# Performance work log

Measured on AMD Instinct MI355X. Metric: run time of the kernel, lower is better.

## Reference

```python
import jax, jax.numpy as jnp
import numpy as np

# Representative causal-LM config (pre-LN GPT/Llama-style, eager attention)
L, D, H, FF, V = 2, 2048, 16, 8192, 32000
B, S = 2, 1024
DH = D // H
NEG = -1e9


def setup_inputs() -> dict:
    key = jax.random.key(0)
    ks = jax.random.split(key, 10)
    p = lambda k, shape: jax.random.normal(k, shape, dtype=jnp.float32) * 0.02
    return {
        "input_ids": jax.random.randint(ks[0], (B, S), 0, V),
        "attention_mask": jnp.ones((B, S), dtype=jnp.int32),
        "emb": p(ks[1], (V, D)),
        "ln1_g": jnp.ones((L, D)), "ln1_b": jnp.zeros((L, D)),
        "Wqkv": p(ks[2], (L, D, 3 * D)),
        "Wo": p(ks[3], (L, D, D)),
        "ln2_g": jnp.ones((L, D)), "ln2_b": jnp.zeros((L, D)),
        "W1": p(ks[4], (L, D, FF)), "W2": p(ks[5], (L, FF, D)),
        "lnf_g": jnp.ones((D,)), "lnf_b": jnp.zeros((D,)),
        "Wc1": p(ks[6], (D, D)), "bc1": jnp.zeros((D,)),
        "Wc2": p(ks[7], (D, 2)), "bc2": jnp.zeros((2,)),
    }


def _ln(x, g, b):
    m = x.mean(-1, keepdims=True)
    v = ((x - m) ** 2).mean(-1, keepdims=True)
    return (x - m) * jax.lax.rsqrt(v + 1e-5) * g + b


def _transformer_reward(input_ids, attention_mask, emb, ln1_g, ln1_b, Wqkv, Wo,
                        ln2_g, ln2_b, W1, W2, lnf_g, lnf_b, Wc1, bc1, Wc2, bc2):
    x = emb[input_ids]                                  # [B,S,D] embedding lookup
    causal = jnp.tril(jnp.ones((S, S), dtype=bool))     # [S,S]
    pad = attention_mask.astype(bool)[:, None, None, :] # [B,1,1,S]
    bias = jnp.where(causal[None, None] & pad, 0.0, NEG).astype(jnp.float32)
    scale = 1.0 / np.sqrt(DH).astype(np.float32)
    for l in range(L):
        h = _ln(x, ln1_g[l], ln1_b[l])
        qkv = h @ Wqkv[l]                               # [B,S,3D]
        q, k, v = jnp.split(qkv, 3, axis=-1)
        q = q.reshape(B, S, H, DH).transpose(0, 2, 1, 3)
        k = k.reshape(B, S, H, DH).transpose(0, 2, 1, 3)
        v = v.reshape(B, S, H, DH).transpose(0, 2, 1, 3)
        # eager attention: full [B,H,S,S] score matrix (as in attn_implementation='eager')
        scores = jnp.einsum('bhqd,bhkd->bhqk', q, k) * scale + bias
        attn = jax.nn.softmax(scores, axis=-1)
        o = jnp.einsum('bhqk,bhkd->bhqd', attn, v).transpose(0, 2, 1, 3).reshape(B, S, D)
        x = x + o @ Wo[l]
        h = _ln(x, ln2_g[l], ln2_b[l])
        x = x + jax.nn.gelu(h @ W1[l]) @ W2[l]
    hs = _ln(x, lnf_g, lnf_b)                           # hidden_states[-1]
    m = attention_mask[:, :, None].astype(jnp.float32)
    mean = (hs * m).sum(axis=1) / jnp.clip(m.sum(axis=1), 1e-9)  # masked mean pool
    logits = jnp.tanh(mean @ Wc1 + bc1) @ Wc2 + bc2     # classifier head
    return jax.nn.softmax(logits, axis=-1)[:, 1]        # rewards [B]


def reference(input_ids, attention_mask, emb, ln1_g, ln1_b, Wqkv, Wo,
              ln2_g, ln2_b, W1, W2, lnf_g, lnf_b, Wc1, bc1, Wc2, bc2):
    return _transformer_reward(input_ids, attention_mask, emb, ln1_g, ln1_b, Wqkv, Wo,
                               ln2_g, ln2_b, W1, W2, lnf_g, lnf_b, Wc1, bc1, Wc2, bc2)
```

## Files before the change

kernel.cpp:

```cpp
#include <hip/hip_runtime.h>
#include <hip/hip_bf16.h>

using bf16 = __hip_bfloat16;
typedef short s16x8 __attribute__((ext_vector_type(8)));
typedef float f32x4 __attribute__((ext_vector_type(4)));

static constexpr int D  = 2048;
static constexpr int H  = 16;
static constexpr int FF = 8192;
static constexpr int S  = 1024;
static constexpr int NB = 2;
static constexpr int DH = 128;
static constexpr int L  = 2;
static constexpr int BS = NB * S;
static constexpr int BH = NB * H;
static constexpr int D3 = 3 * D;

__device__ __forceinline__ float wave_sum(float v) {
#pragma unroll
  for (int o = 32; o > 0; o >>= 1) v += __shfl_down(v, o, 64);
  return v;
}
__device__ __forceinline__ float wave_max(float v) {
#pragma unroll
  for (int o = 32; o > 0; o >>= 1) v = fmaxf(v, __shfl_down(v, o, 64));
  return v;
}

__device__ __forceinline__ void gll16(const void* g, void* l) {
  __builtin_amdgcn_global_load_lds(
      (const __attribute__((address_space(1))) unsigned int*)g,
      (__attribute__((address_space(3))) unsigned int*)l, 16, 0, 0);
}

__device__ __forceinline__ float gelu_tanh(float x) {
  return 0.5f * x * (1.0f + tanhf(0.7978845608028654f * (x + 0.044715f * x * x * x)));
}

__device__ __forceinline__ void stv(float* p, long i, float v) { p[i] = v; }
__device__ __forceinline__ void stv(bf16* p, long i, float v)  { p[i] = __float2bfloat16(v); }

template <int EPI>
__launch_bounds__(256)
__global__ void gemm_k(const bf16* __restrict__ A, int lda, long sAb, long sAh,
                       const bf16* __restrict__ Bt, int ldb, long sBb, long sBh,
                       void* __restrict__ Cp, int ldc, long sCb, long sCh,
                       const float* __restrict__ resid, int K, int nH) {
  __shared__ __align__(16) bf16 lsA[2][128 * 32];
  __shared__ __align__(16) bf16 lsB[2][128 * 32];
  const int tid = threadIdx.x;
  const int zb = blockIdx.z / nH, zh = blockIdx.z % nH;
  const int m0 = blockIdx.y * 128, n0 = blockIdx.x * 128;
  const int sr = tid >> 2, sc = (tid & 3) * 8;
  const bf16* Ag = A + zb * sAb + zh * sAh + (long)(m0 + sr) * lda + sc;
  const bf16* Bg = Bt + zb * sBb + zh * sBh + (long)(n0 + sr) * ldb + sc;
  const long a64 = 64L * lda, b64 = 64L * ldb;

  const int lane = tid & 63, wv = tid >> 6;
  const int wm = (wv >> 1) * 64, wn = (wv & 1) * 64;
  const int fl = lane & 15, fg = lane >> 4;

  f32x4 acc[4][4];
#pragma unroll
  for (int i = 0; i < 4; i++)
#pragma unroll
    for (int j = 0; j < 4; j++) acc[i][j] = (f32x4){0.f, 0.f, 0.f, 0.f};

  gll16(Ag, lsA[0] + tid * 8);
  gll16(Ag + a64, lsA[0] + 2048 + tid * 8);
  gll16(Bg, lsB[0] + tid * 8);
  gll16(Bg + b64, lsB[0] + 2048 + tid * 8);
  __syncthreads();

  int it = 0;
  for (int k0 = 0; k0 < K; k0 += 32, it ^= 1) {
    const int nxt = it ^ 1;
    if (k0 + 32 < K) {
      gll16(Ag + k0 + 32, lsA[nxt] + tid * 8);
      gll16(Ag + a64 + k0 + 32, lsA[nxt] + 2048 + tid * 8);
      gll16(Bg + k0 + 32, lsB[nxt] + tid * 8);
      gll16(Bg + b64 + k0 + 32, lsB[nxt] + 2048 + tid * 8);
    }
    s16x8 af[4], bq[4];
#pragma unroll
    for (int i = 0; i < 4; i++) {
      af[i] = *(const s16x8*)(lsA[it] + (wm + i * 16 + fl) * 32 + fg * 8);
      bq[i] = *(const s16x8*)(lsB[it] + (wn + i * 16 + fl) * 32 + fg * 8);
    }
#pragma unroll
    for (int i = 0; i < 4; i++)
#pragma unroll
      for (int j = 0; j < 4; j++)
        acc[i][j] = __builtin_amdgcn_mfma_f32_16x16x32_bf16(af[i], bq[j], acc[i][j], 0, 0, 0);
    __syncthreads();
  }

  const long offC = zb * sCb + zh * sCh;
#pragma unroll
  for (int i = 0; i < 4; i++) {
#pragma unroll
    for (int j = 0; j < 4; j++) {
      const int row = m0 + wm + i * 16 + fg * 4;
      const int col = n0 + wn + j * 16 + fl;
#pragma unroll
      for (int r = 0; r < 4; r++) {
        const long ci = offC + (long)(row + r) * ldc + col;
        float v = acc[i][j][r];
        if (EPI == 0) {
          ((float*)Cp)[ci] = v;
        } else if (EPI == 1) {
          ((bf16*)Cp)[ci] = __float2bfloat16(v);
        } else if (EPI == 2) {
          ((float*)Cp)[ci] = v + resid[ci];
        } else {
          ((bf16*)Cp)[ci] = __float2bfloat16(gelu_tanh(v));
        }
      }
    }
  }
}

template <int EPI>
__launch_bounds__(512, 2)
__global__ void gemm256_k(const bf16* __restrict__ A, int lda, long sAb, long sAh,
                          const bf16* __restrict__ Bt, int ldb, long sBb, long sBh,
                          void* __restrict__ Cp, int ldc, long sCb, long sCh,
                          int K, int nH) {
  __shared__ __align__(16) bf16 lsA[2][256 * 64];
  __shared__ __align__(16) bf16 lsB[2][256 * 64];
  const int tid = threadIdx.x;
  const int zb = blockIdx.z / nH, zh = blockIdx.z % nH;
  const int m0 = blockIdx.y * 256, n0 = blockIdx.x * 256;

  const int sr = tid >> 3;
  const int sc = (tid & 7) ^ (sr & 7);
  const bf16* Ag = A + zb * sAb + zh * sAh + (long)(m0 + sr) * lda + sc * 8;
  const bf16* Bg = Bt + zb * sBb + zh * sBh +
                   (long)(n0 + (tid >> 8) * 64 + (sr & 31)) * ldb + sc * 8;

  const int lane = tid & 63, wv = tid >> 6;
  const int wm = wv >> 2;
  const int wn = wv & 3;
  const int fl = lane & 15, fg = lane >> 4;

  const int aob = (wm * 64 + fl) * 64;
  const int bob = (wn * 32 + fl) * 64;
  const int s0 = ((fg) ^ (fl & 7)) * 8;
  const int s1 = ((4 + fg) ^ (fl & 7)) * 8;

  s16x8 a[4][2];
  s16x8 bq[2][2][2];
  f32x4 acc[2][4][2][2];
#pragma unroll
  for (int qm = 0; qm < 2; qm++)
#pragma unroll
    for (int mf = 0; mf < 4; mf++)
#pragma unroll
      for (int qn = 0; qn < 2; qn++)
#pragma unroll
        for (int nf = 0; nf < 2; nf++) acc[qm][mf][qn][nf] = (f32x4){0.f, 0.f, 0.f, 0.f};

#define STAGE_A(buf, qm, kt)                                                  \
  do {                                                                        \
    const bf16* _s = Ag + (long)((qm) * 64) * lda + (kt) * 64;                \
    gll16(_s, lsA[buf] + (qm) * 8192 + tid * 8);                              \
    gll16(_s + 128L * lda, lsA[buf] + (qm) * 8192 + 4096 + tid * 8);          \
  } while (0)
#define STAGE_B(buf, qn, kt)                                                  \
  do {                                                                        \
    const bf16* _s = Bg + (long)((qn) * 32) * ldb + (kt) * 64;                \
    gll16(_s, lsB[buf] + (qn) * 8192 + tid * 8);                              \
    gll16(_s + 128L * ldb, lsB[buf] + (qn) * 8192 + 4096 + tid * 8);          \
  } while (0)
#define LDA8(buf, qm)                                                         \
  do {                                                                        \
    const bf16* _p = lsA[buf] + (qm) * 8192 + aob;                            \
    a[0][0] = *(const s16x8*)(_p + s0);        a[0][1] = *(const s16x8*)(_p + s1);        \
    a[1][0] = *(const s16x8*)(_p + 1024 + s0); a[1][1] = *(const s16x8*)(_p + 1024 + s1); \
    a[2][0] = *(const s16x8*)(_p + 2048 + s0); a[2][1] = *(const s16x8*)(_p + 2048 + s1); \
    a[3][0] = *(const s16x8*)(_p + 3072 + s0); a[3][1] = *(const s16x8*)(_p + 3072 + s1); \
  } while (0)
#define LDB4(buf, qn)                                                         \
  do {                                                                        \
    const bf16* _p = lsB[buf] + (qn) * 8192 + bob;                            \
    bq[qn][0][0] = *(const s16x8*)(_p + s0);        bq[qn][0][1] = *(const s16x8*)(_p + s1);        \
    bq[qn][1][0] = *(const s16x8*)(_p + 1024 + s0); bq[qn][1][1] = *(const s16x8*)(_p + 1024 + s1); \
  } while (0)
#define MM16(qm, qn)                                                          \
  do {                                                                        \
    _Pragma("unroll") for (int mf = 0; mf < 4; ++mf) {                        \
      acc[qm][mf][qn][0] = __builtin_amdgcn_mfma_f32_16x16x32_bf16(           \
          a[mf][0], bq[qn][0][0], acc[qm][mf][qn][0], 0, 0, 0);               \
      acc[qm][mf][qn][1] = __builtin_amdgcn_mfma_f32_16x16x32_bf16(           \
          a[mf][0], bq[qn][1][0], acc[qm][mf][qn][1], 0, 0, 0);               \
      acc[qm][mf][qn][0] = __builtin_amdgcn_mfma_f32_16x16x32_bf16(           \
          a[mf][1], bq[qn][0][1], acc[qm][mf][qn][0], 0, 0, 0);               \
      acc[qm][mf][qn][1] = __builtin_amdgcn_mfma_f32_16x16x32_bf16(           \
          a[mf][1], bq[qn][1][1], acc[qm][mf][qn][1], 0, 0, 0);               \
    }                                                                         \
  } while (0)
#define PHASE_TAIL(qm, qn)                                                    \
  __builtin_amdgcn_s_barrier();                                               \
  asm volatile("s_waitcnt lgkmcnt(0)" ::: "memory");                          \
  __builtin_amdgcn_sched_barrier(0);                                          \
  __builtin_amdgcn_s_setprio(1);                                              \
  MM16(qm, qn);                                                               \
  __builtin_amdgcn_s_setprio(0);

  const int NT = K >> 6;

  STAGE_A(0, 0, 0); STAGE_B(0, 0, 0); STAGE_B(0, 1, 0); STAGE_A(0, 1, 0);
  STAGE_A(1, 0, 1); STAGE_B(1, 0, 1); STAGE_B(1, 1, 1);
  asm volatile("s_waitcnt vmcnt(6)" ::: "memory");
  __builtin_amdgcn_s_barrier();

  for (int t = 0; t < NT; t += 2) {
    const bool nl = (t + 2 < NT);
    LDA8(0, 0);
    LDB4(0, 0);
    STAGE_A(1, 1, t + 1);
    PHASE_TAIL(0, 0);
    __builtin_amdgcn_s_barrier();
    LDB4(0, 1);
    if (nl) STAGE_A(0, 0, t + 2);
    PHASE_TAIL(0, 1);
    __builtin_amdgcn_s_barrier();
    LDA8(0, 1);
    if (nl) STAGE_B(0, 0, t + 2);
    PHASE_TAIL(1, 0);
    __builtin_amdgcn_s_barrier();
    if (nl) STAGE_B(0, 1, t + 2);
    PHASE_TAIL(1, 1);
    if (nl) asm volatile("s_waitcnt vmcnt(6)" ::: "memory");
    else    asm volatile("s_waitcnt vmcnt(0)" ::: "memory");
    __builtin_amdgcn_s_barrier();
    LDA8(1, 0);
    LDB4(1, 0);
    if (nl) STAGE_A(0, 1, t + 2);
    PHASE_TAIL(0, 0);
    __builtin_amdgcn_s_barrier();
    LDB4(1, 1);
    if (nl) STAGE_A(1, 0, t + 3);
    PHASE_TAIL(0, 1);
    __builtin_amdgcn_s_barrier();
    LDA8(1, 1);
    if (nl) STAGE_B(1, 0, t + 3);
    PHASE_TAIL(1, 0);
    __builtin_amdgcn_s_barrier();
    if (nl) STAGE_B(1, 1, t + 3);
    PHASE_TAIL(1, 1);
    if (nl) asm volatile("s_waitcnt vmcnt(6)" ::: "memory");
    __builtin_amdgcn_s_barrier();
  }

  const long offC = zb * sCb + zh * sCh;
#pragma unroll
  for (int qm = 0; qm < 2; qm++) {
#pragma unroll
    for (int mf = 0; mf < 4; mf++) {
#pragma unroll
      for (int qn = 0; qn < 2; qn++) {
#pragma unroll
        for (int nf = 0; nf < 2; nf++) {
          const int row = m0 + wm * 128 + qm * 64 + mf * 16 + fg * 4;
          const int col = n0 + wn * 64 + qn * 32 + nf * 16 + fl;
#pragma unroll
          for (int r = 0; r < 4; r++) {
            const long ci = offC + (long)(row + r) * ldc + col;
            float v = acc[qm][mf][qn][nf][r];
            if (EPI == 0) {
              ((float*)Cp)[ci] = v;
            } else if (EPI == 1) {
              ((bf16*)Cp)[ci] = __float2bfloat16(v);
            } else {
              ((bf16*)Cp)[ci] = __float2bfloat16(gelu_tanh(v));
            }
          }
        }
      }
    }
  }
#undef STAGE_A
#undef STAGE_B
#undef LDA8
#undef LDB4
#undef MM16
#undef PHASE_TAIL
}

__launch_bounds__(256)
__global__ void reduce4_k(const float* __restrict__ p, float* __restrict__ x) {
  const long i = (long)blockIdx.x * 256 + threadIdx.x;
  const long n = (long)BS * D / 4;
  const float4 a = ((const float4*)p)[i];
  const float4 b = ((const float4*)p)[i + n];
  const float4 c = ((const float4*)p)[i + 2 * n];
  const float4 d2 = ((const float4*)p)[i + 3 * n];
  float4 xv = ((float4*)x)[i];
  xv.x += a.x + b.x + c.x + d2.x;
  xv.y += a.y + b.y + c.y + d2.y;
  xv.z += a.z + b.z + c.z + d2.z;
  xv.w += a.w + b.w + c.w + d2.w;
  ((float4*)x)[i] = xv;
}

__launch_bounds__(256)
__global__ void transcast_k(const float* __restrict__ in, bf16* __restrict__ out,
                            int R, int C) {
  __shared__ float tile[32][33];
  const int tx = threadIdx.x, ty = threadIdx.y;
  const int c0 = blockIdx.x * 32, r0 = blockIdx.y * 32;
#pragma unroll
  for (int k = 0; k < 4; k++)
    tile[ty + 8 * k][tx] = in[(long)(r0 + ty + 8 * k) * C + c0 + tx];
  __syncthreads();
#pragma unroll
  for (int k = 0; k < 4; k++)
    out[(long)(c0 + ty + 8 * k) * R + r0 + tx] = __float2bfloat16(tile[tx][ty + 8 * k]);
}

__launch_bounds__(256)
__global__ void vtrans_k(const bf16* __restrict__ qkv, bf16* __restrict__ Vt) {
  __shared__ bf16 tile[32][33];
  const int z = blockIdx.z, b = z / H, h = z % H;
  const int d0 = blockIdx.x * 32, s0 = blockIdx.y * 32;
  const int tx = threadIdx.x, ty = threadIdx.y;
#pragma unroll
  for (int k = 0; k < 4; k++)
    tile[ty + 8 * k][tx] =
        qkv[(long)(b * S + s0 + ty + 8 * k) * D3 + 2 * D + h * DH + d0 + tx];
  __syncthreads();
#pragma unroll
  for (int k = 0; k < 4; k++)
    Vt[((long)z * DH + d0 + ty + 8 * k) * S + s0 + tx] = tile[tx][ty + 8 * k];
}

template <typename OutT>
__launch_bounds__(256)
__global__ void ln_k(const float* __restrict__ x, const float* __restrict__ g,
                     const float* __restrict__ bb, OutT* __restrict__ out) {
  __shared__ float sA[4], sB[4];
  const long row = blockIdx.x;
  const int tid = threadIdx.x;
  const float4* xr = (const float4*)(x + row * D);
  float4 v0 = xr[tid], v1 = xr[tid + 256];
  float s = v0.x + v0.y + v0.z + v0.w + v1.x + v1.y + v1.z + v1.w;
  float ss = v0.x * v0.x + v0.y * v0.y + v0.z * v0.z + v0.w * v0.w +
             v1.x * v1.x + v1.y * v1.y + v1.z * v1.z + v1.w * v1.w;
  s = wave_sum(s);
  ss = wave_sum(ss);
  const int lane = tid & 63, wv = tid >> 6;
  if (lane == 0) { sA[wv] = s; sB[wv] = ss; }
  __syncthreads();
  s = sA[0] + sA[1] + sA[2] + sA[3];
  ss = sB[0] + sB[1] + sB[2] + sB[3];
  const float mean = s * (1.f / D);
  const float var = ss * (1.f / D) - mean * mean;
  const float rstd = rsqrtf(var + 1e-5f);
  const float4* gv = (const float4*)g;
  const float4* bv = (const float4*)bb;
  float4 g0 = gv[tid], g1 = gv[tid + 256], c0 = bv[tid], c1 = bv[tid + 256];
  OutT* orow = out + row * D;
  stv(orow, 4 * tid + 0, (v0.x - mean) * rstd * g0.x + c0.x);
  stv(orow, 4 * tid + 1, (v0.y - mean) * rstd * g0.y + c0.y);
  stv(orow, 4 * tid + 2, (v0.z - mean) * rstd * g0.z + c0.z);
  stv(orow, 4 * tid + 3, (v0.w - mean) * rstd * g0.w + c0.w);
  stv(orow, 1024 + 4 * tid + 0, (v1.x - mean) * rstd * g1.x + c1.x);
  stv(orow, 1024 + 4 * tid + 1, (v1.y - mean) * rstd * g1.y + c1.y);
  stv(orow, 1024 + 4 * tid + 2, (v1.z - mean) * rstd * g1.z + c1.z);
  stv(orow, 1024 + 4 * tid + 3, (v1.w - mean) * rstd * g1.w + c1.w);
}

__launch_bounds__(256)
__global__ void embed_k(const int* __restrict__ ids, const float* __restrict__ emb,
                        float* __restrict__ x) {
  const long gid = (long)blockIdx.x * 256 + threadIdx.x;
  const int tok = (int)(gid >> 9);
  const int c = (int)(gid & 511);
  const int id = ids[tok];
  ((float4*)x)[gid] = ((const float4*)(emb + (long)id * D))[c];
}

__launch_bounds__(256)
__global__ void softmax_k(float* __restrict__ scores, const int* __restrict__ amask,
                          float scale) {
  __shared__ float sred[4];
  const int q = blockIdx.x, z = blockIdx.y, b = z / H;
  float* row = scores + ((long)z * S + q) * S;
  const int tid = threadIdx.x;
  const int lane = tid & 63, wv = tid >> 6;
  float v[4];
  float mx = -3.4e38f;
#pragma unroll
  for (int i = 0; i < 4; i++) {
    const int k = tid + i * 256;
    const float s = row[k] * scale;
    const bool ok = (k <= q) && (amask[b * S + k] != 0);
    v[i] = s + (ok ? 0.f : -1e9f);
    mx = fmaxf(mx, v[i]);
  }
  mx = wave_max(mx);
  if (lane == 0) sred[wv] = mx;
  __syncthreads();
  mx = fmaxf(fmaxf(sred[0], sred[1]), fmaxf(sred[2], sred[3]));
  __syncthreads();
  float e[4], sm = 0.f;
#pragma unroll
  for (int i = 0; i < 4; i++) {
    e[i] = __expf(v[i] - mx);
    sm += e[i];
  }
  sm = wave_sum(sm);
  if (lane == 0) sred[wv] = sm;
  __syncthreads();
  sm = sred[0] + sred[1] + sred[2] + sred[3];
  const float inv = 1.f / sm;
  bf16* orow = (bf16*)row;
#pragma unroll
  for (int i = 0; i < 4; i++) orow[tid + i * 256] = __float2bfloat16(e[i] * inv);
}

__launch_bounds__(256)
__global__ void pool_k(const float* __restrict__ hs, const int* __restrict__ amask,
                       float* __restrict__ pooled) {
  const int d = blockIdx.x * 256 + threadIdx.x;
  const int b = blockIdx.y;
  float s = 0.f, cnt = 0.f;
  for (int i = 0; i < S; i++) {
    const float m = (float)amask[b * S + i];
    s += hs[((long)(b * S + i)) * D + d] * m;
    cnt += m;
  }
  pooled[b * D + d] = s / fmaxf(cnt, 1e-9f);
}

__launch_bounds__(256)
__global__ void head1_k(const float* __restrict__ pooled, const float* __restrict__ Wc1,
                        const float* __restrict__ bc1, float* __restrict__ t) {
  const int j = blockIdx.x * 256 + threadIdx.x;
  const int b = blockIdx.y;
  float s = bc1[j];
  for (int d = 0; d < D; d++) s += pooled[b * D + d] * Wc1[(long)d * D + j];
  t[b * D + j] = tanhf(s);
}

__launch_bounds__(256)
__global__ void head2_k(const float* __restrict__ t, const float* __restrict__ Wc2,
                        const float* __restrict__ bc2, float* __restrict__ out) {
  __shared__ float red[4][4];
  const int tid = threadIdx.x;
  const int lane = tid & 63, wv = tid >> 6;
  float a[4] = {0.f, 0.f, 0.f, 0.f};
  for (int j = tid; j < D; j += 256) {
    const float w0 = Wc2[j * 2 + 0], w1 = Wc2[j * 2 + 1];
    const float t0 = t[j], t1 = t[D + j];
    a[0] += t0 * w0; a[1] += t0 * w1; a[2] += t1 * w0; a[3] += t1 * w1;
  }
#pragma unroll
  for (int c = 0; c < 4; c++) a[c] = wave_sum(a[c]);
  if (lane == 0) {
#pragma unroll
    for (int c = 0; c < 4; c++) red[wv][c] = a[c];
  }
  __syncthreads();
  if (tid == 0) {
    float tot[4];
#pragma unroll
    for (int c = 0; c < 4; c++) tot[c] = red[0][c] + red[1][c] + red[2][c] + red[3][c];
    const float l00 = tot[0] + bc2[0], l01 = tot[1] + bc2[1];
    const float l10 = tot[2] + bc2[0], l11 = tot[3] + bc2[1];
    out[0] = 1.f / (1.f + __expf(l00 - l01));
    out[1] = 1.f / (1.f + __expf(l10 - l11));
  }
}

extern "C" void kernel_launch(void* const* d_in, const int* in_sizes, int n_in,
                              void* d_out, int out_size, void* d_ws, size_t ws_size,
                              hipStream_t stream) {
  (void)in_sizes; (void)n_in; (void)out_size; (void)ws_size;
  const int*   ids   = (const int*)d_in[0];
  const int*   amask = (const int*)d_in[1];
  const float* emb   = (const float*)d_in[2];
  const float* ln1g  = (const float*)d_in[3];
  const float* ln1b  = (const float*)d_in[4];
  const float* Wqkv  = (const float*)d_in[5];
  const float* Wo    = (const float*)d_in[6];
  const float* ln2g  = (const float*)d_in[7];
  const float* ln2b  = (const float*)d_in[8];
  const float* W1    = (const float*)d_in[9];
  const float* W2    = (const float*)d_in[10];
  const float* lnfg  = (const float*)d_in[11];
  const float* lnfb  = (const float*)d_in[12];
  const float* Wc1   = (const float*)d_in[13];
  const float* bc1   = (const float*)d_in[14];
  const float* Wc2   = (const float*)d_in[15];
  const float* bc2   = (const float*)d_in[16];
  float* out = (float*)d_out;

  char* ws = (char*)d_ws;
  size_t off = 0;
  auto alloc = [&](size_t bytes) {
    size_t r = off;
    off += (bytes + 255) & ~(size_t)255;
    return r;
  };
  bf16* Wqkv_t = (bf16*)(ws + alloc((size_t)D3 * D * 2));
  bf16* Wo_t   = (bf16*)(ws + alloc((size_t)D * D * 2));
  bf16* W1_t   = (bf16*)(ws + alloc((size_t)FF * D * 2));
  bf16* W2_t   = (bf16*)(ws + alloc((size_t)D * FF * 2));
  float* x     = (float*)(ws + alloc((size_t)BS * D * 4));
  bf16* h      = (bf16*)(ws + alloc((size_t)BS * D * 2));
  bf16* qkv    = (bf16*)(ws + alloc((size_t)BS * D3 * 2));
  bf16* Vt     = (bf16*)(ws + alloc((size_t)BH * DH * S * 2));
  bf16* o_buf  = (bf16*)(ws + alloc((size_t)BS * D * 2));
  float* pooled= (float*)(ws + alloc((size_t)NB * D * 4));
  float* tb    = (float*)(ws + alloc((size_t)NB * D * 4));
  char* big    = ws + alloc((size_t)BH * S * S * 4);
  float* scores = (float*)big;
  bf16*  ffb    = (bf16*)big;
  float* hs     = (float*)big;
  float* parts  = (float*)(big + ((size_t)BS * FF * 2 + 255 & ~(size_t)255));

  const float scale = 0.088388347648318447f;
  dim3 blk(256);
  dim3 blk5(512);
  dim3 tblk(32, 8);

  embed_k<<<4096, blk, 0, stream>>>(ids, emb, x);

  for (int l = 0; l < L; l++) {
    transcast_k<<<dim3(D3 / 32, D / 32), tblk, 0, stream>>>(Wqkv + (size_t)l * D * D3, Wqkv_t, D, D3);
    transcast_k<<<dim3(D / 32, D / 32), tblk, 0, stream>>>(Wo + (size_t)l * D * D, Wo_t, D, D);
    transcast_k<<<dim3(FF / 32, D / 32), tblk, 0, stream>>>(W1 + (size_t)l * D * FF, W1_t, D, FF);
    transcast_k<<<dim3(D / 32, FF / 32), tblk, 0, stream>>>(W2 + (size_t)l * FF * D, W2_t, FF, D);

    ln_k<bf16><<<BS, blk, 0, stream>>>(x, ln1g + (size_t)l * D, ln1b + (size_t)l * D, h);
    gemm256_k<1><<<dim3(D3 / 256, BS / 256, 1), blk5, 0, stream>>>(
        h, D, 0, 0, Wqkv_t, D, 0, 0, qkv, D3, 0, 0, D, 1);
    vtrans_k<<<dim3(DH / 32, S / 32, BH), tblk, 0, stream>>>(qkv, Vt);
    gemm_k<0><<<dim3(S / 128, S / 128, BH), blk, 0, stream>>>(
        qkv, D3, (long)S * D3, DH,
        qkv + D, D3, (long)S * D3, DH,
        scores, S, (long)H * S * S, (long)S * S, nullptr, DH, H);
    softmax_k<<<dim3(S, BH), blk, 0, stream>>>(scores, amask, scale);
    gemm_k<1><<<dim3(DH / 128, S / 128, BH), blk, 0, stream>>>(
        (const bf16*)scores, 2 * S, (long)H * 2 * S * S, (long)2 * S * S,
        Vt, S, (long)H * DH * S, (long)DH * S,
        o_buf, D, (long)S * D, DH, nullptr, S, H);
    gemm_k<2><<<dim3(D / 128, BS / 128, 1), blk, 0, stream>>>(
        o_buf, D, 0, 0, Wo_t, D, 0, 0, x, D, 0, 0, x, D, 1);
    ln_k<bf16><<<BS, blk, 0, stream>>>(x, ln2g + (size_t)l * D, ln2b + (size_t)l * D, h);
    gemm256_k<3><<<dim3(FF / 256, BS / 256, 1), blk5, 0, stream>>>(
        h, D, 0, 0, W1_t, D, 0, 0, ffb, FF, 0, 0, D, 1);
    gemm256_k<0><<<dim3(D / 256, BS / 256, 4), blk5, 0, stream>>>(
        ffb, FF, 0, 2048, W2_t, FF, 0, 2048,
        parts, D, 0, (long)BS * D, 2048, 4);
    reduce4_k<<<dim3(BS * D / 4 / 256), blk, 0, stream>>>(parts, x);
  }

  ln_k<float><<<BS, blk, 0, stream>>>(x, lnfg, lnfb, hs);
  pool_k<<<dim3(D / 256, NB), blk, 0, stream>>>(hs, amask, pooled);
  head1_k<<<dim3(D / 256, NB), blk, 0, stream>>>(pooled, Wc1, bc1, tb);
  head2_k<<<1, blk, 0, stream>>>(tb, Wc2, bc2, out);
}
```

Before: 1.660 ms.

## Replace eager attention with fused causal flash-attention kernel

Swaps the QK^T GEMM, the separate softmax kernel and the PV GEMM for a single flash-attention kernel. It uses an online softmax over 128-wide KV tiles, XOR-swizzled LDS tiles, and loops only up to the diagonal tile, so blocks above the causal diagonal are skipped. This removes the full fp32 score matrix round trip through HBM and roughly halves the attention FLOPs. The costs are heavy LDS use (64KB+), several block-level syncs per tile, and a grid of only 256 blocks with uneven work per block. The MFMA loop order in the GEMM macro is also reordered.

```diff
diff --git a/kernel.cpp b/kernel.cpp
--- a/kernel.cpp
+++ b/kernel.cpp
@@ -21,9 +21,18 @@
   for (int o = 32; o > 0; o >>= 1) v += __shfl_down(v, o, 64);
   return v;
 }
-__device__ __forceinline__ float wave_max(float v) {
-#pragma unroll
-  for (int o = 32; o > 0; o >>= 1) v = fmaxf(v, __shfl_down(v, o, 64));
+__device__ __forceinline__ float grp_max16(float v) {
+  v = fmaxf(v, __shfl_xor(v, 1));
+  v = fmaxf(v, __shfl_xor(v, 2));
+  v = fmaxf(v, __shfl_xor(v, 4));
+  v = fmaxf(v, __shfl_xor(v, 8));
+  return v;
+}
+__device__ __forceinline__ float grp_sum16(float v) {
+  v += __shfl_xor(v, 1);
+  v += __shfl_xor(v, 2);
+  v += __shfl_xor(v, 4);
+  v += __shfl_xor(v, 8);
   return v;
 }
 
@@ -39,6 +48,10 @@
 
 __device__ __forceinline__ void stv(float* p, long i, float v) { p[i] = v; }
 __device__ __forceinline__ void stv(bf16* p, long i, float v)  { p[i] = __float2bfloat16(v); }
+
+__device__ __forceinline__ s16x8 ldfrag(const bf16* base, int row, int ch) {
+  return *(const s16x8*)(base + row * 128 + ((ch ^ (row & 7)) * 8));
+}
 
 template <int EPI>
 __launch_bounds__(256)
@@ -188,16 +201,18 @@
   } while (0)
 #define MM16(qm, qn)                                                          \
   do {                                                                        \
-    _Pragma("unroll") for (int mf = 0; mf < 4; ++mf) {                        \
+    _Pragma("unroll") for (int mf = 0; mf < 4; ++mf)                          \
       acc[qm][mf][qn][0] = __builtin_amdgcn_mfma_f32_16x16x32_bf16(           \
           a[mf][0], bq[qn][0][0], acc[qm][mf][qn][0], 0, 0, 0);               \
+    _Pragma("unroll") for (int mf = 0; mf < 4; ++mf)                          \
       acc[qm][mf][qn][1] = __builtin_amdgcn_mfma_f32_16x16x32_bf16(           \
           a[mf][0], bq[qn][1][0], acc[qm][mf][qn][1], 0, 0, 0);               \
+    _Pragma("unroll") for (int mf = 0; mf < 4; ++mf)                          \
       acc[qm][mf][qn][0] = __builtin_amdgcn_mfma_f32_16x16x32_bf16(           \
           a[mf][1], bq[qn][0][1], acc[qm][mf][qn][0], 0, 0, 0);               \
+    _Pragma("unroll") for (int mf = 0; mf < 4; ++mf)                          \
       acc[qm][mf][qn][1] = __builtin_amdgcn_mfma_f32_16x16x32_bf16(           \
           a[mf][1], bq[qn][1][1], acc[qm][mf][qn][1], 0, 0, 0);               \
-    }                                                                         \
   } while (0)
 #define PHASE_TAIL(qm, qn)                                                    \
   __builtin_amdgcn_s_barrier();                                               \
@@ -289,6 +304,203 @@
 }
 
 __launch_bounds__(256)
+__global__ void fa_k(const bf16* __restrict__ qkv, const bf16* __restrict__ Vt,
+                     const int* __restrict__ amask, bf16* __restrict__ o_buf,
+                     float scale) {
+  __shared__ __align__(16) bf16 lsQ[128 * 128];
+  __shared__ __align__(16) bf16 lsK[128 * 128];
+  __shared__ __align__(16) bf16 lsV[128 * 128];
+  __shared__ __align__(16) bf16 lsP[128 * 128];
+  __shared__ float smx[2][128];
+  __shared__ float sms[2][128];
+
+  const int tid = threadIdx.x;
+  const int qi = blockIdx.x, z = blockIdx.y, b = z / H, h = z % H;
+  const int q0 = qi * 128;
+  const int lane = tid & 63, wv = tid >> 6;
+  const int wm = (wv >> 1) * 64, wn = (wv & 1) * 64;
+  const int wnb = wn >> 6;
+  const int fl = lane & 15, fg = lane >> 4;
+
+  const int sr = tid >> 4;
+  const int scc = (tid & 15) ^ (sr & 7);
+  const bf16* Qg = qkv + (long)(b * S + q0 + sr) * D3 + h * DH + scc * 8;
+  const bf16* Kg = qkv + (long)(b * S + sr) * D3 + D + h * DH + scc * 8;
+  const bf16* Vg = Vt + ((long)z * DH + sr) * S + scc * 8;
+
+#define STAGE_Q()                                                             \
+  do { _Pragma("unroll") for (int g = 0; g < 8; g++)                          \
+    gll16(Qg + (long)g * 16 * D3, lsQ + g * 2048 + tid * 8); } while (0)
+#define STAGE_KT(kv0)                                                         \
+  do { _Pragma("unroll") for (int g = 0; g < 8; g++)                          \
+    gll16(Kg + (long)((kv0) + g * 16) * D3, lsK + g * 2048 + tid * 8); } while (0)
+#define STAGE_VT(kv0)                                                         \
+  do { _Pragma("unroll") for (int g = 0; g < 8; g++)                          \
+    gll16(Vg + (long)g * 16 * S + (kv0), lsV + g * 2048 + tid * 8); } while (0)
+
+  f32x4 o_acc[4][4];
+#pragma unroll
+  for (int i = 0; i < 4; i++)
+#pragma unroll
+    for (int j = 0; j < 4; j++) o_acc[i][j] = (f32x4){0.f, 0.f, 0.f, 0.f};
+  float m_st[4][4], l_st[4][4];
+#pragma unroll
+  for (int i = 0; i < 4; i++)
+#pragma unroll
+    for (int r = 0; r < 4; r++) { m_st[i][r] = -1e30f; l_st[i][r] = 0.f; }
+
+  STAGE_Q();
+  STAGE_KT(0);
+  STAGE_VT(0);
+
+  for (int t = 0; t <= qi; ++t) {
+    const int kv0 = t * 128;
+    asm volatile("s_waitcnt vmcnt(0)" ::: "memory");
+    __syncthreads();
+
+    f32x4 s_acc[4][4];
+#pragma unroll
+    for (int i = 0; i < 4; i++)
+#pragma unroll
+      for (int j = 0; j < 4; j++) s_acc[i][j] = (f32x4){0.f, 0.f, 0.f, 0.f};
+#pragma unroll
+    for (int kk = 0; kk < 4; kk++) {
+      s16x8 qa[4], kb[4];
+#pragma unroll
+      for (int i = 0; i < 4; i++) qa[i] = ldfrag(lsQ, wm + i * 16 + fl, kk * 4 + fg);
+#pragma unroll
+      for (int j = 0; j < 4; j++) kb[j] = ldfrag(lsK, wn + j * 16 + fl, kk * 4 + fg);
+#pragma unroll
+      for (int i = 0; i < 4; i++)
+#pragma unroll
+        for (int j = 0; j < 4; j++)
+          s_acc[i][j] = __builtin_amdgcn_mfma_f32_16x16x32_bf16(qa[i], kb[j], s_acc[i][j], 0, 0, 0);
+    }
+
+    int am[4];
+#pragma unroll
+    for (int j = 0; j < 4; j++) am[j] = amask[b * S + kv0 + wn + j * 16 + fl];
+#pragma unroll
+    for (int i = 0; i < 4; i++)
+#pragma unroll
+      for (int j = 0; j < 4; j++)
+#pragma unroll
+        for (int r = 0; r < 4; r++) {
+          const int row = q0 + wm + i * 16 + fg * 4 + r;
+          const int col = kv0 + wn + j * 16 + fl;
+          const bool ok = (col <= row) && (am[j] != 0);
+          s_acc[i][j][r] = s_acc[i][j][r] * scale + (ok ? 0.f : -1e9f);
+        }
+
+    float pm[4][4];
+#pragma unroll
+    for (int i = 0; i < 4; i++)
+#pragma unroll
+      for (int r = 0; r < 4; r++) {
+        float v = fmaxf(fmaxf(s_acc[i][0][r], s_acc[i][1][r]),
+                        fmaxf(s_acc[i][2][r], s_acc[i][3][r]));
+        pm[i][r] = grp_max16(v);
+      }
+    if (fl == 0) {
+#pragma unroll
+      for (int i = 0; i < 4; i++)
+#pragma unroll
+        for (int r = 0; r < 4; r++) smx[wnb][wm + i * 16 + fg * 4 + r] = pm[i][r];
+    }
+    __syncthreads();
+    if (t < qi) STAGE_KT(kv0 + 128);
+
+    float al[4][4];
+#pragma unroll
+    for (int i = 0; i < 4; i++)
+#pragma unroll
+      for (int r = 0; r < 4; r++) {
+        const float other = smx[wnb ^ 1][wm + i * 16 + fg * 4 + r];
+        const float tm = fmaxf(pm[i][r], other);
+        const float mn = fmaxf(m_st[i][r], tm);
+        al[i][r] = __expf(m_st[i][r] - mn);
+        m_st[i][r] = mn;
+      }
+
+    float ps[4][4];
+#pragma unroll
+    for (int i = 0; i < 4; i++)
+#pragma unroll
+      for (int r = 0; r < 4; r++) {
+        float sm = 0.f;
+#pragma unroll
+        for (int j = 0; j < 4; j++) {
+          s_acc[i][j][r] = __expf(s_acc[i][j][r] - m_st[i][r]);
+          sm += s_acc[i][j][r];
+        }
+        ps[i][r] = grp_sum16(sm);
+      }
+    if (fl == 0) {
+#pragma unroll
+      for (int i = 0; i < 4; i++)
+#pragma unroll
+        for (int r = 0; r < 4; r++) sms[wnb][wm + i * 16 + fg * 4 + r] = ps[i][r];
+    }
+    __syncthreads();
+
+#pragma unroll
+    for (int i = 0; i < 4; i++)
+#pragma unroll
+      for (int r = 0; r < 4; r++) {
+        const float other = sms[wnb ^ 1][wm + i * 16 + fg * 4 + r];
+        l_st[i][r] = l_st[i][r] * al[i][r] + ps[i][r] + other;
+#pragma unroll
+        for (int j = 0; j < 4; j++) o_acc[i][j][r] *= al[i][r];
+      }
+#pragma unroll
+    for (int i = 0; i < 4; i++)
+#pragma unroll
+      for (int j = 0; j < 4; j++)
+#pragma unroll
+        for (int r = 0; r < 4; r++) {
+          const int prow = wm + i * 16 + fg * 4 + r;
+          const int pcol = wn + j * 16 + fl;
+          const int ch = pcol >> 3;
+          lsP[prow * 128 + ((ch ^ (prow & 7)) * 8) + (pcol & 7)] =
+              __float2bfloat16(s_acc[i][j][r]);
+        }
+    __syncthreads();
+
+#pragma unroll
+    for (int kk = 0; kk < 4; kk++) {
+      s16x8 pa[4], vb[4];
+#pragma unroll
+      for (int i = 0; i < 4; i++) pa[i] = ldfrag(lsP, wm + i * 16 + fl, kk * 4 + fg);
+#pragma unroll
+      for (int j = 0; j < 4; j++) vb[j] = ldfrag(lsV, wn + j * 16 + fl, kk * 4 + fg);
+#pragma unroll
+      for (int i = 0; i < 4; i++)
+#pragma unroll
+        for (int j = 0; j < 4; j++)
+          o_acc[i][j] = __builtin_amdgcn_mfma_f32_16x16x32_bf16(pa[i], vb[j], o_acc[i][j], 0, 0, 0);
+    }
+    __syncthreads();
+    if (t < qi) STAGE_VT(kv0 + 128);
+  }
+
+#pragma unroll
+  for (int i = 0; i < 4; i++)
+#pragma unroll
+    for (int r = 0; r < 4; r++) {
+      const float inv = 1.f / l_st[i][r];
+      const int row = q0 + wm + i * 16 + fg * 4 + r;
+#pragma unroll
+      for (int j = 0; j < 4; j++) {
+        const int col = h * DH + wn + j * 16 + fl;
+        o_buf[(long)(b * S + row) * D + col] = __float2bfloat16(o_acc[i][j][r] * inv);
+      }
+    }
+#undef STAGE_Q
+#undef STAGE_KT
+#undef STAGE_VT
+}
+
+__launch_bounds__(256)
 __global__ void reduce4_k(const float* __restrict__ p, float* __restrict__ x) {
   const long i = (long)blockIdx.x * 256 + threadIdx.x;
   const long n = (long)BS * D / 4;
@@ -382,45 +594,6 @@
 }
 
 __launch_bounds__(256)
-__global__ void softmax_k(float* __restrict__ scores, const int* __restrict__ amask,
-                          float scale) {
-  __shared__ float sred[4];
-  const int q = blockIdx.x, z = blockIdx.y, b = z / H;
-  float* row = scores + ((long)z * S + q) * S;
-  const int tid = threadIdx.x;
-  const int lane = tid & 63, wv = tid >> 6;
-  float v[4];
-  float mx = -3.4e38f;
-#pragma unroll
-  for (int i = 0; i < 4; i++) {
-    const int k = tid + i * 256;
-    const float s = row[k] * scale;
-    const bool ok = (k <= q) && (amask[b * S + k] != 0);
-    v[i] = s + (ok ? 0.f : -1e9f);
-    mx = fmaxf(mx, v[i]);
-  }
-  mx = wave_max(mx);
-  if (lane == 0) sred[wv] = mx;
-  __syncthreads();
-  mx = fmaxf(fmaxf(sred[0], sred[1]), fmaxf(sred[2], sred[3]));
-  __syncthreads();
-  float e[4], sm = 0.f;
-#pragma unroll
-  for (int i = 0; i < 4; i++) {
-    e[i] = __expf(v[i] - mx);
-    sm += e[i];
-  }
-  sm = wave_sum(sm);
-  if (lane == 0) sred[wv] = sm;
-  __syncthreads();
-  sm = sred[0] + sred[1] + sred[2] + sred[3];
-  const float inv = 1.f / sm;
-  bf16* orow = (bf16*)row;
-#pragma unroll
-  for (int i = 0; i < 4; i++) orow[tid + i * 256] = __float2bfloat16(e[i] * inv);
-}
-
-__launch_bounds__(256)
 __global__ void pool_k(const float* __restrict__ hs, const int* __restrict__ amask,
                        float* __restrict__ pooled) {
   const int d = blockIdx.x * 256 + threadIdx.x;
@@ -516,7 +689,6 @@
   float* pooled= (float*)(ws + alloc((size_t)NB * D * 4));
   float* tb    = (float*)(ws + alloc((size_t)NB * D * 4));
   char* big    = ws + alloc((size_t)BH * S * S * 4);
-  float* scores = (float*)big;
   bf16*  ffb    = (bf16*)big;
   float* hs     = (float*)big;
   float* parts  = (float*)(big + ((size_t)BS * FF * 2 + 255 & ~(size_t)255));
@@ -538,15 +710,7 @@
     gemm256_k<1><<<dim3(D3 / 256, BS / 256, 1), blk5, 0, stream>>>(
         h, D, 0, 0, Wqkv_t, D, 0, 0, qkv, D3, 0, 0, D, 1);
     vtrans_k<<<dim3(DH / 32, S / 32, BH), tblk, 0, stream>>>(qkv, Vt);
-    gemm_k<0><<<dim3(S / 128, S / 128, BH), blk, 0, stream>>>(
-        qkv, D3, (long)S * D3, DH,
-        qkv + D, D3, (long)S * D3, DH,
-        scores, S, (long)H * S * S, (long)S * S, nullptr, DH, H);
-    softmax_k<<<dim3(S, BH), blk, 0, stream>>>(scores, amask, scale);
-    gemm_k<1><<<dim3(DH / 128, S / 128, BH), blk, 0, stream>>>(
-        (const bf16*)scores, 2 * S, (long)H * 2 * S * S, (long)2 * S * S,
-        Vt, S, (long)H * DH * S, (long)DH * S,
-        o_buf, D, (long)S * D, DH, nullptr, S, H);
+    fa_k<<<dim3(S / 128, BH), blk, 0, stream>>>(qkv, Vt, amask, o_buf, scale);
     gemm_k<2><<<dim3(D / 128, BS / 128, 1), blk, 0, stream>>>(
         o_buf, D, 0, 0, Wo_t, D, 0, 0, x, D, 0, 0, x, D, 1);
     ln_k<bf16><<<BS, blk, 0, stream>>>(x, ln2g + (size_t)l * D, ln2b + (size_t)l * D, h);
```

After: 1.604 ms. 3.4% less time.
